# Optimization experiments

Hardware: AMD Instinct MI355X
Metric: run time of the kernel (lower is better)

## Reference

```python
import jax, jax.numpy as jnp
import numpy as np

N, A, R = 131072, 16, 64


def setup_inputs() -> dict:
    key = jax.random.key(0)
    k1, k2, k3 = jax.random.split(key, 3)
    x = jax.random.normal(k1, (N, A), dtype=jnp.float32)
    mu = jax.random.uniform(k2, (R, A), dtype=jnp.float32)      # torch.rand(R, A)
    sigma = jnp.ones((R, A), dtype=jnp.float32) * 0.2           # torch.ones(R, A) * 0.2
    rho = jax.random.normal(k3, (R, A + 1), dtype=jnp.float32) * 0.1
    return {"x": x, "mu": mu, "sigma": sigma, "rho": rho}


def reference(x, mu, sigma, rho):
    # Rule consequents: z[k, r] = x[k] . rho[r, :A] + rho[r, A]   -> [N, R]
    z = jnp.einsum("na,ra->nr", x, rho[:, :-1]) + rho[:, -1]
    # Gaussian membership firing strengths (prod of exps == exp of sum):
    # w[k, r] = prod_a exp(-(x[k,a]-mu[r,a])^2 / (2 sigma[r,a]^2))
    d = x[:, None, :] - mu[None, :, :]                           # [N, R, A]
    logw = -jnp.sum(d * d / (2.0 * sigma[None] ** 2), axis=-1)   # [N, R]
    w = jnp.exp(logw)
    # diag(z @ w.T)[k] = sum_r z[k,r] * w[k,r]; normalized by rule-sum.
    num = jnp.sum(z * w, axis=1)
    den = jnp.sum(w, axis=1) + 1e-13
    return num / den
```

## Files before the change

kernel.cpp:

```cpp
#include <hip/hip_runtime.h>
#include <math.h>

#define NFEAT 16
#define NRULE 64
#define TPW 2

typedef _Float16 half8 __attribute__((ext_vector_type(8)));
typedef float    f4    __attribute__((ext_vector_type(4)));
union F4H8 { float4 f; half8 h; };

__global__ __launch_bounds__(256, 3) void fuzzy_fused(const float* __restrict__ x,
                                                      const float* __restrict__ mu,
                                                      const float* __restrict__ sigma,
                                                      const float* __restrict__ rho,
                                                      float* __restrict__ out, int n) {
    const float L2E = 1.4426950408889634f;
    const int tid  = threadIdx.x;
    const int L    = tid & 63;
    const int quad = L >> 4;
    const int m    = L & 15;
    const int wv   = __builtin_amdgcn_readfirstlane(tid >> 6);
    const int fb   = (quad & 1) * 8;

    const int tbase = (blockIdx.x * 4 + wv) * TPW;
    float4 xa[TPW], xb[TPW];
#pragma unroll
    for (int t = 0; t < TPW; ++t) {
        int tb = (tbase + t) * 16;
        int sc = tb + m < n ? tb + m : n - 1;
        const float4* xp = (const float4*)(x + (size_t)sc * NFEAT + fb);
        xa[t] = xp[0]; xb[t] = xp[1];
    }

    F4H8 c1[4], c2[4], b1[4], b2[4], r1[4], r2[4];
    float Kv[4], Bv[4];
#pragma unroll
    for (int T = 0; T < 4; ++T) {
        int rule = T * 16 + m;
        const float* mrow = mu    + rule * NFEAT + fb;
        const float* srow = sigma + rule * NFEAT + fb;
        const float* rrow = rho   + rule * (NFEAT + 1) + fb;
        float kp = 0.0f;
#pragma unroll
        for (int j = 0; j < 8; ++j) {
            float mm = mrow[j], ss = srow[j], rr = rrow[j];
            float iv = __builtin_amdgcn_rcpf(2.0f * ss * ss);
            float Cw = -iv * L2E;
            _Float16 ch = (_Float16)Cw;
            c1[T].h[j] = ch;
            c2[T].h[j] = (_Float16)(Cw - (float)ch);
            float Bw = 2.0f * iv * mm * L2E;
            _Float16 bh = (_Float16)Bw;
            b1[T].h[j] = bh;
            b2[T].h[j] = (_Float16)(Bw - (float)bh);
            _Float16 rh_ = (_Float16)rr;
            r1[T].h[j] = rh_;
            r2[T].h[j] = (_Float16)(rr - (float)rh_);
            kp = fmaf(iv * mm, mm, kp);
        }
        Kv[T] = -(kp + __shfl_xor(kp, 16)) * L2E;
        Bv[T] = rho[rule * (NFEAT + 1) + NFEAT];
    }

#pragma unroll
    for (int t = 0; t < TPW; ++t) {
        int tb = (tbase + t) * 16;
        if (tb >= n) break;
        float xv[8] = {xa[t].x, xa[t].y, xa[t].z, xa[t].w,
                       xb[t].x, xb[t].y, xb[t].z, xb[t].w};
        F4H8 a1, a2;
#pragma unroll
        for (int j = 0; j < 8; ++j) {
            float v = xv[j];
            _Float16 h = (_Float16)v;
            a1.h[j] = (quad < 2) ? h : (_Float16)(v - (float)h);
            float s = v * v;
            _Float16 hs = (_Float16)s;
            a2.h[j] = (quad < 2) ? hs : (_Float16)(s - (float)hs);
        }

        f4 nsum = {0.f, 0.f, 0.f, 0.f}, dsum = {0.f, 0.f, 0.f, 0.f};
#pragma unroll
        for (int T = 0; T < 4; ++T) {
            f4 z4 = {0.f, 0.f, 0.f, 0.f};
            f4 accG = __builtin_amdgcn_mfma_f32_16x16x32_f16(a2.h, c1[T].h, z4, 0, 0, 0);
            accG    = __builtin_amdgcn_mfma_f32_16x16x32_f16(a2.h, c2[T].h, accG, 0, 0, 0);
            accG    = __builtin_amdgcn_mfma_f32_16x16x32_f16(a1.h, b1[T].h, accG, 0, 0, 0);
            accG    = __builtin_amdgcn_mfma_f32_16x16x32_f16(a1.h, b2[T].h, accG, 0, 0, 0);
            f4 accZ = __builtin_amdgcn_mfma_f32_16x16x32_f16(a1.h, r1[T].h, z4, 0, 0, 0);
            accZ    = __builtin_amdgcn_mfma_f32_16x16x32_f16(a1.h, r2[T].h, accZ, 0, 0, 0);
#pragma unroll
            for (int p = 0; p < 4; ++p) {
                float l = accG[p] + Kv[T];
                float w = __builtin_amdgcn_exp2f(l);
                float zf = accZ[p] + Bv[T];
                nsum[p] = fmaf(zf, w, nsum[p]);
                dsum[p] += w;
            }
        }
#pragma unroll
        for (int d = 1; d < 16; d <<= 1) {
#pragma unroll
            for (int p = 0; p < 4; ++p) {
                nsum[p] += __shfl_xor(nsum[p], d);
                dsum[p] += __shfl_xor(dsum[p], d);
            }
        }
        if (m == 0) {
            float4 o;
            o.x = nsum[0] * __builtin_amdgcn_rcpf(dsum[0] + 1e-13f);
            o.y = nsum[1] * __builtin_amdgcn_rcpf(dsum[1] + 1e-13f);
            o.z = nsum[2] * __builtin_amdgcn_rcpf(dsum[2] + 1e-13f);
            o.w = nsum[3] * __builtin_amdgcn_rcpf(dsum[3] + 1e-13f);
            ((float4*)(out + tb))[quad] = o;
        }
    }
}

extern "C" void kernel_launch(void* const* d_in, const int* in_sizes, int n_in,
                              void* d_out, int out_size, void* d_ws, size_t ws_size,
                              hipStream_t stream) {
    const float* x     = (const float*)d_in[0];
    const float* mu    = (const float*)d_in[1];
    const float* sigma = (const float*)d_in[2];
    const float* rho   = (const float*)d_in[3];
    float* out = (float*)d_out;

    int n = in_sizes[0] / NFEAT;

    int blocks = (n + 16 * 4 * TPW - 1) / (16 * 4 * TPW);
    fuzzy_fused<<<blocks, 256, 0, stream>>>(x, mu, sigma, rho, out, n);
}
```

Measured before the change: 77.32 us.

## Split rule coefficients into two phases to cut registers and raise occupancy

Rule coefficient fragments are now built in two phases of 32 rules, each immediately consumed by the MFMA work for both tiles, instead of holding all 64 rules' fp16 split coefficients live at once. Input fragments are converted up front and partial sums are kept per tile across phases. Launch bounds rise from 3 to 4 waves per SIMD to use the lower register pressure. The cost is recomputing the coefficients in a serial loop with extra loads, and keeping accumulators for both tiles live.

```diff
diff --git a/kernel.cpp b/kernel.cpp
--- a/kernel.cpp
+++ b/kernel.cpp
@@ -2,14 +2,13 @@
 #include <math.h>
 
 #define NFEAT 16
-#define NRULE 64
 #define TPW 2
 
 typedef _Float16 half8 __attribute__((ext_vector_type(8)));
 typedef float    f4    __attribute__((ext_vector_type(4)));
 union F4H8 { float4 f; half8 h; };
 
-__global__ __launch_bounds__(256, 3) void fuzzy_fused(const float* __restrict__ x,
+__global__ __launch_bounds__(256, 4) void fuzzy_fused(const float* __restrict__ x,
                                                       const float* __restrict__ mu,
                                                       const float* __restrict__ sigma,
                                                       const float* __restrict__ rho,
@@ -23,95 +22,107 @@
     const int fb   = (quad & 1) * 8;
 
     const int tbase = (blockIdx.x * 4 + wv) * TPW;
-    float4 xa[TPW], xb[TPW];
+
+    F4H8 a1[TPW], a2[TPW];
 #pragma unroll
     for (int t = 0; t < TPW; ++t) {
         int tb = (tbase + t) * 16;
         int sc = tb + m < n ? tb + m : n - 1;
         const float4* xp = (const float4*)(x + (size_t)sc * NFEAT + fb);
-        xa[t] = xp[0]; xb[t] = xp[1];
+        float4 va = xp[0], vb = xp[1];
+        float xv[8] = {va.x, va.y, va.z, va.w, vb.x, vb.y, vb.z, vb.w};
+#pragma unroll
+        for (int j = 0; j < 8; ++j) {
+            float v = xv[j];
+            _Float16 h = (_Float16)v;
+            a1[t].h[j] = (quad < 2) ? h : (_Float16)(v - (float)h);
+            float s = v * v;
+            _Float16 hs = (_Float16)s;
+            a2[t].h[j] = (quad < 2) ? hs : (_Float16)(s - (float)hs);
+        }
     }
 
-    F4H8 c1[4], c2[4], b1[4], b2[4], r1[4], r2[4];
-    float Kv[4], Bv[4];
+    f4 nsum[TPW], dsum[TPW];
 #pragma unroll
-    for (int T = 0; T < 4; ++T) {
-        int rule = T * 16 + m;
-        const float* mrow = mu    + rule * NFEAT + fb;
-        const float* srow = sigma + rule * NFEAT + fb;
-        const float* rrow = rho   + rule * (NFEAT + 1) + fb;
-        float kp = 0.0f;
+    for (int t = 0; t < TPW; ++t) {
+        nsum[t] = (f4){0.f, 0.f, 0.f, 0.f};
+        dsum[t] = (f4){0.f, 0.f, 0.f, 0.f};
+    }
+
+#pragma unroll 1
+    for (int ph = 0; ph < 2; ++ph) {
+        F4H8 c1[2], c2[2], b1[2], b2[2], r1[2], r2[2];
+        float Kv[2], Bv[2];
 #pragma unroll
-        for (int j = 0; j < 8; ++j) {
-            float mm = mrow[j], ss = srow[j], rr = rrow[j];
-            float iv = __builtin_amdgcn_rcpf(2.0f * ss * ss);
-            float Cw = -iv * L2E;
-            _Float16 ch = (_Float16)Cw;
-            c1[T].h[j] = ch;
-            c2[T].h[j] = (_Float16)(Cw - (float)ch);
-            float Bw = 2.0f * iv * mm * L2E;
-            _Float16 bh = (_Float16)Bw;
-            b1[T].h[j] = bh;
-            b2[T].h[j] = (_Float16)(Bw - (float)bh);
-            _Float16 rh_ = (_Float16)rr;
-            r1[T].h[j] = rh_;
-            r2[T].h[j] = (_Float16)(rr - (float)rh_);
-            kp = fmaf(iv * mm, mm, kp);
+        for (int T2 = 0; T2 < 2; ++T2) {
+            int rule = (ph * 2 + T2) * 16 + m;
+            const float* mrow = mu    + rule * NFEAT + fb;
+            const float* srow = sigma + rule * NFEAT + fb;
+            const float* rrow = rho   + rule * (NFEAT + 1) + fb;
+            float kp = 0.0f;
+#pragma unroll
+            for (int j = 0; j < 8; ++j) {
+                float mm = mrow[j], ss = srow[j], rr = rrow[j];
+                float iv = __builtin_amdgcn_rcpf(2.0f * ss * ss);
+                float Cw = -iv * L2E;
+                _Float16 ch = (_Float16)Cw;
+                c1[T2].h[j] = ch;
+                c2[T2].h[j] = (_Float16)(Cw - (float)ch);
+                float Bw = 2.0f * iv * mm * L2E;
+                _Float16 bh = (_Float16)Bw;
+                b1[T2].h[j] = bh;
+                b2[T2].h[j] = (_Float16)(Bw - (float)bh);
+                _Float16 rh_ = (_Float16)rr;
+                r1[T2].h[j] = rh_;
+                r2[T2].h[j] = (_Float16)(rr - (float)rh_);
+                kp = fmaf(iv * mm, mm, kp);
+            }
+            Kv[T2] = -(kp + __shfl_xor(kp, 16)) * L2E;
+            Bv[T2] = rho[rule * (NFEAT + 1) + NFEAT];
         }
-        Kv[T] = -(kp + __shfl_xor(kp, 16)) * L2E;
-        Bv[T] = rho[rule * (NFEAT + 1) + NFEAT];
+
+#pragma unroll
+        for (int t = 0; t < TPW; ++t) {
+#pragma unroll
+            for (int T2 = 0; T2 < 2; ++T2) {
+                f4 z4 = (f4){0.f, 0.f, 0.f, 0.f};
+                f4 accG = __builtin_amdgcn_mfma_f32_16x16x32_f16(a2[t].h, c1[T2].h, z4, 0, 0, 0);
+                accG    = __builtin_amdgcn_mfma_f32_16x16x32_f16(a2[t].h, c2[T2].h, accG, 0, 0, 0);
+                accG    = __builtin_amdgcn_mfma_f32_16x16x32_f16(a1[t].h, b1[T2].h, accG, 0, 0, 0);
+                accG    = __builtin_amdgcn_mfma_f32_16x16x32_f16(a1[t].h, b2[T2].h, accG, 0, 0, 0);
+                f4 accZ = __builtin_amdgcn_mfma_f32_16x16x32_f16(a1[t].h, r1[T2].h, z4, 0, 0, 0);
+                accZ    = __builtin_amdgcn_mfma_f32_16x16x32_f16(a1[t].h, r2[T2].h, accZ, 0, 0, 0);
+#pragma unroll
+                for (int p = 0; p < 4; ++p) {
+                    float l = accG[p] + Kv[T2];
+                    float w = __builtin_amdgcn_exp2f(l);
+                    float zf = accZ[p] + Bv[T2];
+                    nsum[t][p] = fmaf(zf, w, nsum[t][p]);
+                    dsum[t][p] += w;
+                }
+            }
+        }
     }
 
 #pragma unroll
     for (int t = 0; t < TPW; ++t) {
         int tb = (tbase + t) * 16;
         if (tb >= n) break;
-        float xv[8] = {xa[t].x, xa[t].y, xa[t].z, xa[t].w,
-                       xb[t].x, xb[t].y, xb[t].z, xb[t].w};
-        F4H8 a1, a2;
-#pragma unroll
-        for (int j = 0; j < 8; ++j) {
-            float v = xv[j];
-            _Float16 h = (_Float16)v;
-            a1.h[j] = (quad < 2) ? h : (_Float16)(v - (float)h);
-            float s = v * v;
-            _Float16 hs = (_Float16)s;
-            a2.h[j] = (quad < 2) ? hs : (_Float16)(s - (float)hs);
-        }
-
-        f4 nsum = {0.f, 0.f, 0.f, 0.f}, dsum = {0.f, 0.f, 0.f, 0.f};
-#pragma unroll
-        for (int T = 0; T < 4; ++T) {
-            f4 z4 = {0.f, 0.f, 0.f, 0.f};
-            f4 accG = __builtin_amdgcn_mfma_f32_16x16x32_f16(a2.h, c1[T].h, z4, 0, 0, 0);
-            accG    = __builtin_amdgcn_mfma_f32_16x16x32_f16(a2.h, c2[T].h, accG, 0, 0, 0);
-            accG    = __builtin_amdgcn_mfma_f32_16x16x32_f16(a1.h, b1[T].h, accG, 0, 0, 0);
-            accG    = __builtin_amdgcn_mfma_f32_16x16x32_f16(a1.h, b2[T].h, accG, 0, 0, 0);
-            f4 accZ = __builtin_amdgcn_mfma_f32_16x16x32_f16(a1.h, r1[T].h, z4, 0, 0, 0);
-            accZ    = __builtin_amdgcn_mfma_f32_16x16x32_f16(a1.h, r2[T].h, accZ, 0, 0, 0);
-#pragma unroll
-            for (int p = 0; p < 4; ++p) {
-                float l = accG[p] + Kv[T];
-                float w = __builtin_amdgcn_exp2f(l);
-                float zf = accZ[p] + Bv[T];
-                nsum[p] = fmaf(zf, w, nsum[p]);
-                dsum[p] += w;
-            }
-        }
+        f4 nn = nsum[t], dd = dsum[t];
 #pragma unroll
         for (int d = 1; d < 16; d <<= 1) {
 #pragma unroll
             for (int p = 0; p < 4; ++p) {
-                nsum[p] += __shfl_xor(nsum[p], d);
-                dsum[p] += __shfl_xor(dsum[p], d);
+                nn[p] += __shfl_xor(nn[p], d);
+                dd[p] += __shfl_xor(dd[p], d);
             }
         }
         if (m == 0) {
             float4 o;
-            o.x = nsum[0] * __builtin_amdgcn_rcpf(dsum[0] + 1e-13f);
-            o.y = nsum[1] * __builtin_amdgcn_rcpf(dsum[1] + 1e-13f);
-            o.z = nsum[2] * __builtin_amdgcn_rcpf(dsum[2] + 1e-13f);
-            o.w = nsum[3] * __builtin_amdgcn_rcpf(dsum[3] + 1e-13f);
+            o.x = nn[0] * __builtin_amdgcn_rcpf(dd[0] + 1e-13f);
+            o.y = nn[1] * __builtin_amdgcn_rcpf(dd[1] + 1e-13f);
+            o.z = nn[2] * __builtin_amdgcn_rcpf(dd[2] + 1e-13f);
+            o.w = nn[3] * __builtin_amdgcn_rcpf(dd[3] + 1e-13f);
             ((float4*)(out + tb))[quad] = o;
         }
     }
```

After: 73.35 us. 1.05x faster.
